# Kernel tuning notes

Hardware: AMD Instinct MI355X
Metric: run time of the kernel (lower is better)

Reference implementation:

```python
import jax, jax.numpy as jnp
import numpy as np

BLOCK_SIZES = [256] * 16
LAYER_SIZE = sum(BLOCK_SIZES)  # 4096
N_ROWS = 8192


def _block_diag_mask(sizes):
    m = np.zeros((sum(sizes), sum(sizes)), dtype=bool)
    off = 0
    for s in sizes:
        m[off:off + s, off:off + s] = True
        off += s
    return jnp.asarray(m)


def setup_inputs() -> dict:
    key = jax.random.key(0)
    k1, k2 = jax.random.split(key)
    mask = _block_diag_mask(BLOCK_SIZES)
    # _blocks param: block_diagonal(raw_blocks) -> dense matrix, zero off-block
    blocks = jax.random.normal(k1, (LAYER_SIZE, LAYER_SIZE), dtype=jnp.float32) * mask
    x = jax.random.normal(k2, (N_ROWS, LAYER_SIZE), dtype=jnp.float32)
    return {"x": x, "blocks": blocks, "mask": mask}


def reference(x, blocks, mask):
    # blocks property: mask then tanh (constrained='tanh'); tanh(0)=0 preserves structure
    b = jnp.tanh(blocks * mask)
    # forward: dense matmul x @ blocks (no bias)
    return x @ b
```

## Files before the change

### kernel.cpp

```cpp
#include <hip/hip_runtime.h>
#include <stdint.h>


typedef float floatx4 __attribute__((ext_vector_type(4)));
typedef __bf16 bf16x8 __attribute__((ext_vector_type(8)));

#define LDX 4096
#define NBLK 16
#define BS 256

__device__ __forceinline__ unsigned int f2bf(float f) {
  union { float f; unsigned int i; } x;
  x.f = f;
  unsigned int r = x.i + 0x7FFFu + ((x.i >> 16) & 1u);
  return r >> 16;
}

__device__ __forceinline__ bf16x8 pack8(const float4& a, const float4& b) {
  union { uint4 u; bf16x8 h; } v;
  v.u.x = f2bf(a.x) | (f2bf(a.y) << 16);
  v.u.y = f2bf(a.z) | (f2bf(a.w) << 16);
  v.u.z = f2bf(b.x) | (f2bf(b.y) << 16);
  v.u.w = f2bf(b.z) | (f2bf(b.w) << 16);
  return v.h;
}

__device__ __forceinline__ void async_copy16(const void* g, void* l) {
  __builtin_amdgcn_global_load_lds(
      (__attribute__((address_space(1))) void*)(uintptr_t)g,
      (__attribute__((address_space(3))) void*)(unsigned int)(uintptr_t)l,
      16, 0, 0);
}

#define BWAIT(N)                                              \
  do {                                                        \
    asm volatile("s_waitcnt vmcnt(" #N ")" ::: "memory");     \
    __builtin_amdgcn_s_barrier();                             \
    __builtin_amdgcn_sched_barrier(0);                        \
  } while (0)

__global__ __launch_bounds__(256) void tanh_pack(const float* __restrict__ blocks,
                                                 unsigned short* __restrict__ wsT) {
  __shared__ float tile[64][65];
  const int t = threadIdx.x;
  const int tc = blockIdx.x, tr = blockIdx.y, j = blockIdx.z;
  const float* src = blocks + (size_t)(j * BS + tr * 64) * LDX + j * BS + tc * 64;
#pragma unroll
  for (int it = 0; it < 8; ++it) {
    int v = it * 256 + t;
    int row = v >> 5;
    int c2 = (v & 31) * 2;
    float2 f = *(const float2*)(src + (size_t)row * LDX + c2);
    tile[row][c2] = tanhf(f.x);
    tile[row][c2 + 1] = tanhf(f.y);
  }
  __syncthreads();
  unsigned char* dstj =
      (unsigned char*)wsT + (size_t)j * 131072 + (size_t)tr * 32768;
#pragma unroll
  for (int it = 0; it < 8; ++it) {
    int v = it * 256 + t;
    int nn = v >> 5;
    int k2 = (v & 31) * 2;
    int n = tc * 64 + nn;
    unsigned int pair = f2bf(tile[k2][nn]) | (f2bf(tile[k2 + 1][nn]) << 16);
    unsigned int off = (unsigned)n * 128 + (((unsigned)(k2 * 2)) ^ (((unsigned)(n & 7)) << 4));
    *(unsigned int*)(dstj + off) = pair;
  }
}

__global__ __launch_bounds__(512, 2) void bdgemm2(const float* __restrict__ x,
                                                  const unsigned short* __restrict__ wsT,
                                                  float* __restrict__ out) {
  __shared__ unsigned short Bs[65536];
  const int t = threadIdx.x;
  const int lane = t & 63;
  const int wave = t >> 6;
  const int mg = blockIdx.x;
  const int j = blockIdx.y;

  const int fr = lane & 15;
  const int kq = lane >> 4;
  const int sw = (fr & 7) << 4;
  const int ko0 = ((kq * 16) + 0) ^ sw;
  const int ko1 = ((kq * 16) + 64) ^ sw;

  const float* xg = x + (size_t)(mg * 512 + wave * 32 + fr) * LDX + j * BS + kq * 8;
  char* ldsb = (char*)Bs;

  float4 s0[8], s1[8];
  floatx4 acc[2][16];

  auto issueA = [&](float4* s, int sc) {
#pragma unroll
    for (int kt = 0; kt < 2; ++kt)
#pragma unroll
      for (int mi = 0; mi < 2; ++mi) {
        const float* q = xg + (size_t)((sc >> 2) * 256 + mi * 16) * LDX +
                         (sc & 3) * 64 + kt * 32;
        s[kt * 4 + mi * 2 + 0] = *(const float4*)(q);
        s[kt * 4 + mi * 2 + 1] = *(const float4*)(q + 4);
      }
  };

  auto compute = [&](int c, const float4* s) {
#pragma unroll
    for (int kt = 0; kt < 2; ++kt) {
      bf16x8 af0 = pack8(s[kt * 4 + 0], s[kt * 4 + 1]);
      bf16x8 af1 = pack8(s[kt * 4 + 2], s[kt * 4 + 3]);
      const char* bkt = ldsb + c * 32768 + fr * 128 + (kt ? ko1 : ko0);
#pragma unroll
      for (int ni = 0; ni < 16; ++ni) {
        bf16x8 bf = *(const bf16x8*)(bkt + ni * 2048);
        acc[0][ni] = __builtin_amdgcn_mfma_f32_16x16x32_bf16(af0, bf, acc[0][ni], 0, 0, 0);
        acc[1][ni] = __builtin_amdgcn_mfma_f32_16x16x32_bf16(af1, bf, acc[1][ni], 0, 0, 0);
      }
    }
  };

  auto zacc = [&]() {
#pragma unroll
    for (int a = 0; a < 2; ++a)
#pragma unroll
      for (int b = 0; b < 16; ++b) acc[a][b] = (floatx4){0.f, 0.f, 0.f, 0.f};
  };

  auto store = [&](int mblk) {
    float* op = out + (size_t)(mg * 512 + mblk * 256 + wave * 32 + kq * 4) * LDX +
                j * BS + fr;
#pragma unroll
    for (int mi = 0; mi < 2; ++mi)
#pragma unroll
      for (int ni = 0; ni < 16; ++ni)
#pragma unroll
        for (int r = 0; r < 4; ++r)
          op[(size_t)(mi * 16 + r) * LDX + ni * 16] = acc[mi][ni][r];
  };

  issueA(s0, 0);
  issueA(s1, 1);
  const char* wsj = (const char*)wsT + (size_t)j * 131072;
#pragma unroll
  for (int i = 0; i < 16; ++i)
    async_copy16(wsj + i * 8192 + t * 16, ldsb + i * 8192 + t * 16);

  zacc();
  BWAIT(12); compute(0, s0); issueA(s0, 2);
  BWAIT(16); compute(1, s1); issueA(s1, 3);
  BWAIT(20); compute(2, s0); issueA(s0, 4);
  BWAIT(24); compute(3, s1); issueA(s1, 5);
  store(0);

  zacc();
  compute(0, s0); issueA(s0, 6);
  compute(1, s1); issueA(s1, 7);
  compute(2, s0);
  compute(3, s1);
  store(1);
}

template <int BSTR>
__global__ __launch_bounds__(256) void bdgemm_fused(const float* __restrict__ x,
                                                    const float* __restrict__ bg,
                                                    float* __restrict__ out) {
  __shared__ unsigned short As[64 * 32];
  __shared__ unsigned short Bsf[256 * BSTR];
  const int t = threadIdx.x;
  const int lane = t & 63;
  const int wave = t >> 6;
  const int mtile = blockIdx.x;
  const int j = blockIdx.y;
  const int m0 = mtile * 64;
  const float* xg = x + (size_t)m0 * LDX + j * BS;
  const int srow = t >> 2;
  const int scol = (t & 3) * 8;
  const int wn = wave * 64;
  const int fr = lane & 15;
  const int fq = (lane >> 4) * 8;

  floatx4 acc[4][4];
#pragma unroll
  for (int a = 0; a < 4; ++a)
#pragma unroll
    for (int b = 0; b < 4; ++b) acc[a][b] = (floatx4){0.f, 0.f, 0.f, 0.f};

  for (int kt = 0; kt < 8; ++kt) {
    const int k0 = kt * 32;
    const float* ap = xg + (size_t)srow * LDX + k0 + scol;
    float4 a0 = *(const float4*)(ap);
    float4 a1 = *(const float4*)(ap + 4);
    uint4 pk;
    pk.x = f2bf(a0.x) | (f2bf(a0.y) << 16);
    pk.y = f2bf(a0.z) | (f2bf(a0.w) << 16);
    pk.z = f2bf(a1.x) | (f2bf(a1.y) << 16);
    pk.w = f2bf(a1.z) | (f2bf(a1.w) << 16);
    *(uint4*)(As + t * 8) = pk;
#pragma unroll
    for (int i = 0; i < 32; ++i) {
      const int idx = i * 256 + t;
      const int kk = idx >> 8;
      const int nn = idx & 255;
      float v = tanhf(bg[(size_t)(j * BS + k0 + kk) * LDX + j * BS + nn]);
      Bsf[nn * BSTR + kk] = (unsigned short)f2bf(v);
    }
    __syncthreads();
    bf16x8 af[4], bfm[4];
#pragma unroll
    for (int i = 0; i < 4; ++i) {
      af[i] = *(const bf16x8*)(As + (i * 16 + fr) * 32 + fq);
      bfm[i] = *(const bf16x8*)(Bsf + (wn + i * 16 + fr) * BSTR + fq);
    }
#pragma unroll
    for (int mi = 0; mi < 4; ++mi)
#pragma unroll
      for (int ni = 0; ni < 4; ++ni)
        acc[mi][ni] =
            __builtin_amdgcn_mfma_f32_16x16x32_bf16(af[mi], bfm[ni], acc[mi][ni], 0, 0, 0);
    __syncthreads();
  }
  const int r0 = (lane >> 4) * 4;
  const int ocol = j * BS + wn + fr;
#pragma unroll
  for (int mi = 0; mi < 4; ++mi)
#pragma unroll
    for (int ni = 0; ni < 4; ++ni) {
      float* op = out + (size_t)(m0 + mi * 16 + r0) * LDX + ocol + ni * 16;
#pragma unroll
      for (int r = 0; r < 4; ++r) op[(size_t)r * LDX] = acc[mi][ni][r];
    }
}

extern "C" void kernel_launch(void* const* d_in, const int* in_sizes, int n_in,
                              void* d_out, int out_size, void* d_ws, size_t ws_size,
                              hipStream_t stream) {
  const float* x = (const float*)d_in[0];
  const float* blocks = (const float*)d_in[1];
  float* out = (float*)d_out;

  const size_t need = (size_t)NBLK * BS * BS * sizeof(unsigned short);
  if (d_ws != nullptr && ws_size >= need) {
    unsigned short* wsT = (unsigned short*)d_ws;
    tanh_pack<<<dim3(4, 4, NBLK), 256, 0, stream>>>(blocks, wsT);
    bdgemm2<<<dim3(16, NBLK), 512, 0, stream>>>(x, wsT, out);
  } else {
    bdgemm_fused<40><<<dim3(128, NBLK), 256, 0, stream>>>(x, blocks, out);
  }
}
```

Measured before the change: 307.7 us.

## Stage x tiles through LDS and split block GEMM into 2x4 wave grid

Replaces the per-wave register-staged A path with a version that loads 64-row strips of x, converts them to bf16 and writes them into a swizzled LDS buffer shared by all waves. The 8 waves are arranged as a 2x4 grid over each 64x256 output strip, so each wave holds far fewer accumulators (2x4 fragments instead of 2x16). Loads of the next strip are double-buffered in registers while the current one is computed. The aim is lower register pressure and better latency hiding for this memory-heavy kernel, at the cost of extra LDS traffic and more block-wide barriers per strip.

```diff
diff --git a/kernel.cpp b/kernel.cpp
--- a/kernel.cpp
+++ b/kernel.cpp
@@ -16,28 +16,12 @@
   return r >> 16;
 }
 
-__device__ __forceinline__ bf16x8 pack8(const float4& a, const float4& b) {
-  union { uint4 u; bf16x8 h; } v;
-  v.u.x = f2bf(a.x) | (f2bf(a.y) << 16);
-  v.u.y = f2bf(a.z) | (f2bf(a.w) << 16);
-  v.u.z = f2bf(b.x) | (f2bf(b.y) << 16);
-  v.u.w = f2bf(b.z) | (f2bf(b.w) << 16);
-  return v.h;
-}
-
 __device__ __forceinline__ void async_copy16(const void* g, void* l) {
   __builtin_amdgcn_global_load_lds(
       (__attribute__((address_space(1))) void*)(uintptr_t)g,
       (__attribute__((address_space(3))) void*)(unsigned int)(uintptr_t)l,
       16, 0, 0);
 }
-
-#define BWAIT(N)                                              \
-  do {                                                        \
-    asm volatile("s_waitcnt vmcnt(" #N ")" ::: "memory");     \
-    __builtin_amdgcn_s_barrier();                             \
-    __builtin_amdgcn_sched_barrier(0);                        \
-  } while (0)
 
 __global__ __launch_bounds__(256) void tanh_pack(const float* __restrict__ blocks,
                                                  unsigned short* __restrict__ wsT) {
@@ -69,94 +53,119 @@
   }
 }
 
-__global__ __launch_bounds__(512, 2) void bdgemm2(const float* __restrict__ x,
-                                                  const unsigned short* __restrict__ wsT,
-                                                  float* __restrict__ out) {
+__global__ __launch_bounds__(512) void bdgemm4(const float* __restrict__ x,
+                                               const unsigned short* __restrict__ wsT,
+                                               float* __restrict__ out) {
   __shared__ unsigned short Bs[65536];
+  __shared__ unsigned short As[8192];
   const int t = threadIdx.x;
   const int lane = t & 63;
   const int wave = t >> 6;
+  const int wm = wave >> 2;
+  const int wn = wave & 3;
   const int mg = blockIdx.x;
   const int j = blockIdx.y;
 
   const int fr = lane & 15;
   const int kq = lane >> 4;
   const int sw = (fr & 7) << 4;
-  const int ko0 = ((kq * 16) + 0) ^ sw;
-  const int ko1 = ((kq * 16) + 64) ^ sw;
-
-  const float* xg = x + (size_t)(mg * 512 + wave * 32 + fr) * LDX + j * BS + kq * 8;
-  char* ldsb = (char*)Bs;
-
-  float4 s0[8], s1[8];
-  floatx4 acc[2][16];
-
-  auto issueA = [&](float4* s, int sc) {
-#pragma unroll
-    for (int kt = 0; kt < 2; ++kt)
-#pragma unroll
-      for (int mi = 0; mi < 2; ++mi) {
-        const float* q = xg + (size_t)((sc >> 2) * 256 + mi * 16) * LDX +
-                         (sc & 3) * 64 + kt * 32;
-        s[kt * 4 + mi * 2 + 0] = *(const float4*)(q);
-        s[kt * 4 + mi * 2 + 1] = *(const float4*)(q + 4);
+
+  char* bsb = (char*)Bs;
+  char* asb = (char*)As;
+
+  const float* xrow = x + (size_t)(mg * 512 + wave * 8) * LDX + j * BS + lane * 4;
+
+  float4 ra[8], rb[8];
+  floatx4 acc[2][4];
+
+  auto loadA = [&](float4* r, int strip) {
+#pragma unroll
+    for (int q = 0; q < 8; ++q)
+      r[q] = *(const float4*)(xrow + (size_t)(strip * 64 + q) * LDX);
+  };
+
+  auto packAh = [&](const float4* r, int h) {
+    if ((lane >> 5) == h) {
+      const int kb = 8 * (lane & 31);
+#pragma unroll
+      for (int q = 0; q < 8; ++q) {
+        const int lrow = wave * 8 + q;
+        uint2 d;
+        d.x = f2bf(r[q].x) | (f2bf(r[q].y) << 16);
+        d.y = f2bf(r[q].z) | (f2bf(r[q].w) << 16);
+        *(uint2*)(asb + lrow * 256 + (kb ^ ((lrow & 7) << 4))) = d;
       }
-  };
-
-  auto compute = [&](int c, const float4* s) {
-#pragma unroll
-    for (int kt = 0; kt < 2; ++kt) {
-      bf16x8 af0 = pack8(s[kt * 4 + 0], s[kt * 4 + 1]);
-      bf16x8 af1 = pack8(s[kt * 4 + 2], s[kt * 4 + 3]);
-      const char* bkt = ldsb + c * 32768 + fr * 128 + (kt ? ko1 : ko0);
-#pragma unroll
-      for (int ni = 0; ni < 16; ++ni) {
-        bf16x8 bf = *(const bf16x8*)(bkt + ni * 2048);
-        acc[0][ni] = __builtin_amdgcn_mfma_f32_16x16x32_bf16(af0, bf, acc[0][ni], 0, 0, 0);
-        acc[1][ni] = __builtin_amdgcn_mfma_f32_16x16x32_bf16(af1, bf, acc[1][ni], 0, 0, 0);
+    }
+  };
+
+  auto barrier = [&]() {
+    asm volatile("s_waitcnt lgkmcnt(0)" ::: "memory");
+    __builtin_amdgcn_s_barrier();
+    __builtin_amdgcn_sched_barrier(0);
+  };
+
+  auto compute_half = [&](int h) {
+#pragma unroll
+    for (int kk2 = 0; kk2 < 4; ++kk2) {
+      const int kk = h * 4 + kk2;
+      const int c = kk >> 1;
+      const int kb = (((kk & 1) * 64 + kq * 16) ^ sw);
+      const int ka = ((kk2 * 64 + kq * 16) ^ sw);
+      bf16x8 a0 = *(const bf16x8*)(asb + (wm * 32 + fr) * 256 + ka);
+      bf16x8 a1 = *(const bf16x8*)(asb + (wm * 32 + 16 + fr) * 256 + ka);
+      const char* bb = bsb + c * 32768 + (wn * 64 + fr) * 128 + kb;
+#pragma unroll
+      for (int ni = 0; ni < 4; ++ni) {
+        bf16x8 bf = *(const bf16x8*)(bb + ni * 2048);
+        acc[0][ni] = __builtin_amdgcn_mfma_f32_16x16x32_bf16(a0, bf, acc[0][ni], 0, 0, 0);
+        acc[1][ni] = __builtin_amdgcn_mfma_f32_16x16x32_bf16(a1, bf, acc[1][ni], 0, 0, 0);
       }
     }
   };
 
-  auto zacc = [&]() {
+  auto store = [&](int strip) {
+    float* op0 = out + (size_t)(mg * 512 + strip * 64 + wm * 32 + kq * 4) * LDX +
+                 j * BS + wn * 64 + fr;
+#pragma unroll
+    for (int mi = 0; mi < 2; ++mi)
+#pragma unroll
+      for (int ni = 0; ni < 4; ++ni) {
+        float* op = op0 + (size_t)(mi * 16) * LDX + ni * 16;
+#pragma unroll
+        for (int r = 0; r < 4; ++r) op[(size_t)r * LDX] = acc[mi][ni][r];
+      }
+  };
+
+  loadA(ra, 0);
+  const char* wsj = (const char*)wsT + (size_t)j * 131072;
+#pragma unroll
+  for (int i = 0; i < 16; ++i)
+    async_copy16(wsj + i * 8192 + t * 16, bsb + i * 8192 + t * 16);
+  loadA(rb, 1);
+  packAh(ra, 0);
+  asm volatile("s_waitcnt vmcnt(8)" ::: "memory");
+
+#pragma unroll
+  for (int s = 0; s < 8; ++s) {
+    float4* cur = (s & 1) ? rb : ra;
+    float4* nxt = (s & 1) ? ra : rb;
 #pragma unroll
     for (int a = 0; a < 2; ++a)
 #pragma unroll
-      for (int b = 0; b < 16; ++b) acc[a][b] = (floatx4){0.f, 0.f, 0.f, 0.f};
-  };
-
-  auto store = [&](int mblk) {
-    float* op = out + (size_t)(mg * 512 + mblk * 256 + wave * 32 + kq * 4) * LDX +
-                j * BS + fr;
-#pragma unroll
-    for (int mi = 0; mi < 2; ++mi)
-#pragma unroll
-      for (int ni = 0; ni < 16; ++ni)
-#pragma unroll
-        for (int r = 0; r < 4; ++r)
-          op[(size_t)(mi * 16 + r) * LDX + ni * 16] = acc[mi][ni][r];
-  };
-
-  issueA(s0, 0);
-  issueA(s1, 1);
-  const char* wsj = (const char*)wsT + (size_t)j * 131072;
-#pragma unroll
-  for (int i = 0; i < 16; ++i)
-    async_copy16(wsj + i * 8192 + t * 16, ldsb + i * 8192 + t * 16);
-
-  zacc();
-  BWAIT(12); compute(0, s0); issueA(s0, 2);
-  BWAIT(16); compute(1, s1); issueA(s1, 3);
-  BWAIT(20); compute(2, s0); issueA(s0, 4);
-  BWAIT(24); compute(3, s1); issueA(s1, 5);
-  store(0);
-
-  zacc();
-  compute(0, s0); issueA(s0, 6);
-  compute(1, s1); issueA(s1, 7);
-  compute(2, s0);
-  compute(3, s1);
-  store(1);
+      for (int b = 0; b < 4; ++b) acc[a][b] = (floatx4){0.f, 0.f, 0.f, 0.f};
+    barrier();
+    compute_half(0);
+    barrier();
+    packAh(cur, 1);
+    if (s + 2 < 8) loadA(cur, s + 2);
+    barrier();
+    compute_half(1);
+    store(s);
+    if (s < 7) {
+      barrier();
+      packAh(nxt, 0);
+    }
+  }
 }
 
 template <int BSTR>
@@ -241,7 +250,7 @@
   if (d_ws != nullptr && ws_size >= need) {
     unsigned short* wsT = (unsigned short*)d_ws;
     tanh_pack<<<dim3(4, 4, NBLK), 256, 0, stream>>>(blocks, wsT);
-    bdgemm2<<<dim3(16, NBLK), 512, 0, stream>>>(x, wsT, out);
+    bdgemm4<<<dim3(16, NBLK), 512, 0, stream>>>(x, wsT, out);
   } else {
     bdgemm_fused<40><<<dim3(128, NBLK), 256, 0, stream>>>(x, blocks, out);
   }
```

Result: faster. 298.1 us (-3.1%).

## Split block-diagonal GEMM into smaller tiles with N-halves for more workgroups

Applied to the files above, without the earlier changes.

Replaces the large-tile GEMM, where each 512-thread workgroup covers 512 rows of a 256-wide block with a 128KB LDS copy of B, with a kernel that covers 128 rows and half of the N columns. The grid grows from 256 to 2048 workgroups, each staging only 64KB of B in LDS, which allows higher occupancy (launch bounds 4). The aim is better latency hiding and load balance across CUs. In exchange the B half-block is reloaded from global/L2 by many more workgroups, and the hand-tuned pipelined waitcnt schedule is replaced by one full wait before compute.

```diff
diff --git a/kernel.cpp b/kernel.cpp
--- a/kernel.cpp
+++ b/kernel.cpp
@@ -31,13 +31,6 @@
       (__attribute__((address_space(3))) void*)(unsigned int)(uintptr_t)l,
       16, 0, 0);
 }
-
-#define BWAIT(N)                                              \
-  do {                                                        \
-    asm volatile("s_waitcnt vmcnt(" #N ")" ::: "memory");     \
-    __builtin_amdgcn_s_barrier();                             \
-    __builtin_amdgcn_sched_barrier(0);                        \
-  } while (0)
 
 __global__ __launch_bounds__(256) void tanh_pack(const float* __restrict__ blocks,
                                                  unsigned short* __restrict__ wsT) {
@@ -69,94 +62,71 @@
   }
 }
 
-__global__ __launch_bounds__(512, 2) void bdgemm2(const float* __restrict__ x,
+__global__ __launch_bounds__(512, 4) void bdgemm5(const float* __restrict__ x,
                                                   const unsigned short* __restrict__ wsT,
                                                   float* __restrict__ out) {
-  __shared__ unsigned short Bs[65536];
+  __shared__ unsigned short Bs[32768];
   const int t = threadIdx.x;
   const int lane = t & 63;
   const int wave = t >> 6;
-  const int mg = blockIdx.x;
+  const int bx = blockIdx.x;
+  const int mg = bx >> 1;
+  const int nh = bx & 1;
   const int j = blockIdx.y;
 
   const int fr = lane & 15;
   const int kq = lane >> 4;
   const int sw = (fr & 7) << 4;
-  const int ko0 = ((kq * 16) + 0) ^ sw;
-  const int ko1 = ((kq * 16) + 64) ^ sw;
-
-  const float* xg = x + (size_t)(mg * 512 + wave * 32 + fr) * LDX + j * BS + kq * 8;
-  char* ldsb = (char*)Bs;
-
-  float4 s0[8], s1[8];
-  floatx4 acc[2][16];
-
-  auto issueA = [&](float4* s, int sc) {
-#pragma unroll
-    for (int kt = 0; kt < 2; ++kt)
-#pragma unroll
-      for (int mi = 0; mi < 2; ++mi) {
-        const float* q = xg + (size_t)((sc >> 2) * 256 + mi * 16) * LDX +
-                         (sc & 3) * 64 + kt * 32;
-        s[kt * 4 + mi * 2 + 0] = *(const float4*)(q);
-        s[kt * 4 + mi * 2 + 1] = *(const float4*)(q + 4);
-      }
-  };
-
-  auto compute = [&](int c, const float4* s) {
-#pragma unroll
-    for (int kt = 0; kt < 2; ++kt) {
-      bf16x8 af0 = pack8(s[kt * 4 + 0], s[kt * 4 + 1]);
-      bf16x8 af1 = pack8(s[kt * 4 + 2], s[kt * 4 + 3]);
-      const char* bkt = ldsb + c * 32768 + fr * 128 + (kt ? ko1 : ko0);
-#pragma unroll
-      for (int ni = 0; ni < 16; ++ni) {
-        bf16x8 bf = *(const bf16x8*)(bkt + ni * 2048);
-        acc[0][ni] = __builtin_amdgcn_mfma_f32_16x16x32_bf16(af0, bf, acc[0][ni], 0, 0, 0);
-        acc[1][ni] = __builtin_amdgcn_mfma_f32_16x16x32_bf16(af1, bf, acc[1][ni], 0, 0, 0);
-      }
-    }
-  };
-
-  auto zacc = [&]() {
-#pragma unroll
-    for (int a = 0; a < 2; ++a)
-#pragma unroll
-      for (int b = 0; b < 16; ++b) acc[a][b] = (floatx4){0.f, 0.f, 0.f, 0.f};
-  };
-
-  auto store = [&](int mblk) {
-    float* op = out + (size_t)(mg * 512 + mblk * 256 + wave * 32 + kq * 4) * LDX +
-                j * BS + fr;
-#pragma unroll
-    for (int mi = 0; mi < 2; ++mi)
-#pragma unroll
-      for (int ni = 0; ni < 16; ++ni)
-#pragma unroll
-        for (int r = 0; r < 4; ++r)
-          op[(size_t)(mi * 16 + r) * LDX + ni * 16] = acc[mi][ni][r];
-  };
-
-  issueA(s0, 0);
-  issueA(s1, 1);
-  const char* wsj = (const char*)wsT + (size_t)j * 131072;
-#pragma unroll
-  for (int i = 0; i < 16; ++i)
-    async_copy16(wsj + i * 8192 + t * 16, ldsb + i * 8192 + t * 16);
-
-  zacc();
-  BWAIT(12); compute(0, s0); issueA(s0, 2);
-  BWAIT(16); compute(1, s1); issueA(s1, 3);
-  BWAIT(20); compute(2, s0); issueA(s0, 4);
-  BWAIT(24); compute(3, s1); issueA(s1, 5);
-  store(0);
-
-  zacc();
-  compute(0, s0); issueA(s0, 6);
-  compute(1, s1); issueA(s1, 7);
-  compute(2, s0);
-  compute(3, s1);
-  store(1);
+
+  char* bsb = (char*)Bs;
+
+  const int row = mg * 128 + wave * 16 + fr;
+  const float* ap = x + (size_t)row * LDX + j * BS + kq * 8;
+
+  float4 sa[2][2];
+  sa[0][0] = *(const float4*)(ap);
+  sa[0][1] = *(const float4*)(ap + 4);
+  sa[1][0] = *(const float4*)(ap + 32);
+  sa[1][1] = *(const float4*)(ap + 36);
+
+  const char* wsj = (const char*)wsT + (size_t)j * 131072 + nh * 16384;
+#pragma unroll
+  for (int i = 0; i < 8; ++i) {
+    const int c = i >> 1, h = i & 1;
+    async_copy16(wsj + c * 32768 + h * 8192 + t * 16,
+                 bsb + c * 16384 + h * 8192 + t * 16);
+  }
+  asm volatile("s_waitcnt vmcnt(0)" ::: "memory");
+  __builtin_amdgcn_s_barrier();
+
+  floatx4 acc[8];
+#pragma unroll
+  for (int b = 0; b < 8; ++b) acc[b] = (floatx4){0.f, 0.f, 0.f, 0.f};
+
+#pragma unroll
+  for (int kk = 0; kk < 8; ++kk) {
+    const int sl = kk & 1;
+    bf16x8 af = pack8(sa[sl][0], sa[sl][1]);
+    if (kk + 2 < 8) {
+      sa[sl][0] = *(const float4*)(ap + (kk + 2) * 32);
+      sa[sl][1] = *(const float4*)(ap + (kk + 2) * 32 + 4);
+    }
+    const char* bb =
+        bsb + (kk >> 1) * 16384 + fr * 128 + (((kk & 1) * 64 + kq * 16) ^ sw);
+#pragma unroll
+    for (int ni = 0; ni < 8; ++ni) {
+      bf16x8 bf = *(const bf16x8*)(bb + ni * 2048);
+      acc[ni] = __builtin_amdgcn_mfma_f32_16x16x32_bf16(af, bf, acc[ni], 0, 0, 0);
+    }
+  }
+
+  float* op0 = out + (size_t)(mg * 128 + wave * 16 + kq * 4) * LDX + j * BS +
+               nh * 128 + fr;
+#pragma unroll
+  for (int ni = 0; ni < 8; ++ni)
+#pragma unroll
+    for (int r = 0; r < 4; ++r)
+      op0[(size_t)r * LDX + ni * 16] = acc[ni][r];
 }
 
 template <int BSTR>
@@ -241,7 +211,7 @@
   if (d_ws != nullptr && ws_size >= need) {
     unsigned short* wsT = (unsigned short*)d_ws;
     tanh_pack<<<dim3(4, 4, NBLK), 256, 0, stream>>>(blocks, wsT);
-    bdgemm2<<<dim3(16, NBLK), 512, 0, stream>>>(x, wsT, out);
+    bdgemm5<<<dim3(128, NBLK), 512, 0, stream>>>(x, wsT, out);
   } else {
     bdgemm_fused<40><<<dim3(128, NBLK), 256, 0, stream>>>(x, blocks, out);
   }
```

After: 331.0 us. 1.08x slower.
